# Kernel tuning notes

Measured on AMD Instinct MI355X. Metric: run time of the kernel, lower is better.

The kernel has to match this reference:

```python
import math
import jax, jax.numpy as jnp
import numpy as np

B, L, D, H, V, R, NL = 4, 1024, 1024, 16, 50257, 4, 3
LORA_SCALE = 32.0 / R  # alpha / r
EPS = 1e-5
GELU_C = math.sqrt(2.0 / math.pi)


def gelu(x):
    return 0.5 * x * (1.0 + jnp.tanh(GELU_C * (x + 0.044715 * x ** 3)))


def layer_norm(x, w, b):
    u = x.mean(-1, keepdims=True)
    s = ((x - u) ** 2).mean(-1, keepdims=True)
    return w * (x - u) / jnp.sqrt(s + EPS) + b


def setup_inputs() -> dict:
    key = jax.random.key(0)
    ks = jax.random.split(key, 10)
    std = 0.02
    inp = {
        'input_ids': jax.random.randint(ks[0], (B, L), 0, V),
        'wte': jax.random.normal(ks[1], (V, D), jnp.float32) * std,
        'wpe': jax.random.normal(ks[2], (L, D), jnp.float32) * std,
        'ln1_w': jnp.ones((NL, D), jnp.float32),
        'ln1_b': jnp.zeros((NL, D), jnp.float32),
        'attn_w': jax.random.normal(ks[3], (NL, D, 3 * D), jnp.float32) * std,
        'attn_b': jnp.zeros((NL, 3 * D), jnp.float32),
        'lora_A': jax.random.normal(ks[4], (NL, 2 * R, D), jnp.float32) * std,
        'lora_B': jax.random.normal(ks[5], (NL, 2 * D, R), jnp.float32) * std,
        'proj_w': jax.random.normal(ks[6], (NL, D, D), jnp.float32) * std,
        'proj_b': jnp.zeros((NL, D), jnp.float32),
        'ln2_w': jnp.ones((NL, D), jnp.float32),
        'ln2_b': jnp.zeros((NL, D), jnp.float32),
        'fc_w': jax.random.normal(ks[7], (NL, D, 4 * D), jnp.float32) * std,
        'fc_b': jnp.zeros((NL, 4 * D), jnp.float32),
        'fc2_w': jax.random.normal(ks[8], (NL, 4 * D, D), jnp.float32) * std,
        'fc2_b': jnp.zeros((NL, D), jnp.float32),
    }
    return inp


def block(x, causal, p):
    (ln1w, ln1b, aw, ab, lA, lB, pw, pb, ln2w, ln2b, fw, fb, f2w, f2b) = p
    h = layer_norm(x, ln1w, ln1b)
    # LoRA-merged QKV: base GEMM + low-rank deltas on Q and V groups
    qkv = h @ aw + ab                     # [B,L,3D]
    after_A = h @ lA.T                    # [B,L,2R]
    dq = after_A[..., :R] @ lB[:D].T * LORA_SCALE   # [B,L,D]
    dv = after_A[..., R:] @ lB[D:].T * LORA_SCALE   # [B,L,D]
    q = qkv[..., :D] + dq
    k = qkv[..., D:2 * D]
    v = qkv[..., 2 * D:] + dv
    # split heads -> [B,H,L,hd]
    hd = D // H
    q = q.reshape(B, L, H, hd).transpose(0, 2, 1, 3)
    k = k.reshape(B, L, H, hd).transpose(0, 2, 1, 3)
    v = v.reshape(B, L, H, hd).transpose(0, 2, 1, 3)
    w = jnp.einsum('bhqd,bhkd->bhqk', q, k) / math.sqrt(hd)
    w = w * causal - 1e10 * (1.0 - causal)  # multiplicative causal mask trick
    w = jax.nn.softmax(w, axis=-1)
    a = jnp.einsum('bhqk,bhkd->bhqd', w, v)
    a = a.transpose(0, 2, 1, 3).reshape(B, L, D)
    a = a @ pw + pb
    x = x + a
    m = layer_norm(x, ln2w, ln2b)
    m = gelu(m @ fw + fb) @ f2w + f2b
    return x + m


def reference(input_ids, wte, wpe, ln1_w, ln1_b, attn_w, attn_b, lora_A, lora_B,
              proj_w, proj_b, ln2_w, ln2_b, fc_w, fc_b, fc2_w, fc2_b):
    pos = jnp.arange(L)
    x = wte[input_ids] + wpe[pos][None, :, :]   # [B,L,D]
    causal = jnp.tril(jnp.ones((L, L), x.dtype))
    for i in range(NL):
        p = (ln1_w[i], ln1_b[i], attn_w[i], attn_b[i], lora_A[i], lora_B[i],
             proj_w[i], proj_b[i], ln2_w[i], ln2_b[i], fc_w[i], fc_b[i],
             fc2_w[i], fc2_b[i])
        x = block(x, causal, p)
    return x
```

## Files before the change

### kernel.cpp

```cpp
#include <hip/hip_runtime.h>

typedef __bf16 bf16x8 __attribute__((ext_vector_type(8)));
typedef float f32x4 __attribute__((ext_vector_type(4)));
typedef unsigned short u16x8 __attribute__((ext_vector_type(8)));
typedef unsigned short u16x4 __attribute__((ext_vector_type(4)));
typedef unsigned int u32x4 __attribute__((ext_vector_type(4)));

#define DEV static __device__ __forceinline__

DEV unsigned short f2bf(float f){
  return __builtin_bit_cast(unsigned short, (__bf16)f);
}
DEV float bf2f(unsigned short h){
  return __builtin_bit_cast(float, ((unsigned int)h) << 16);
}
DEV f32x4 bf4_to_f32(u16x4 h){
  f32x4 r = {bf2f(h[0]), bf2f(h[1]), bf2f(h[2]), bf2f(h[3])};
  return r;
}
DEV float gelu_f(float x){
  float z = 0.7978845608028654f * (x + 0.044715f * x * x * x);
  float e = __expf(2.0f * z);
  float th = 1.0f - 2.0f / (e + 1.0f);
  return 0.5f * x * (1.0f + th);
}

#define BAR() do{ asm volatile("" ::: "memory"); __builtin_amdgcn_s_barrier(); asm volatile("" ::: "memory"); }while(0)
#define LGKM0() asm volatile("s_waitcnt lgkmcnt(0)" ::: "memory")

__global__ __launch_bounds__(256)
void prep_weights(const float* __restrict__ attnw, const float* __restrict__ lorA,
                  const float* __restrict__ lorB, const float* __restrict__ projw,
                  const float* __restrict__ fcw, const float* __restrict__ fc2w,
                  unsigned short* __restrict__ WTA, unsigned short* __restrict__ WTP,
                  unsigned short* __restrict__ WTF, unsigned short* __restrict__ WTF2){
  __shared__ float tile[32][33];
  const int blk = blockIdx.x;
  const int layer = blk / 12288;
  const int r = blk % 12288;
  const float* in; unsigned short* out; int R, C, bx, by; bool lora;
  if (r < 3072){
    in = attnw + (size_t)layer*1024*3072; out = WTA + (size_t)layer*3072*1024;
    R = 1024; C = 3072; bx = r % 96; by = r / 96; lora = true;
  } else if (r < 4096){
    int rr = r - 3072;
    in = projw + (size_t)layer*1024*1024; out = WTP + (size_t)layer*1024*1024;
    R = 1024; C = 1024; bx = rr % 32; by = rr / 32; lora = false;
  } else if (r < 8192){
    int rr = r - 4096;
    in = fcw + (size_t)layer*1024*4096; out = WTF + (size_t)layer*4096*1024;
    R = 1024; C = 4096; bx = rr % 128; by = rr / 128; lora = false;
  } else {
    int rr = r - 8192;
    in = fc2w + (size_t)layer*4096*1024; out = WTF2 + (size_t)layer*1024*4096;
    R = 4096; C = 1024; bx = rr % 32; by = rr / 32; lora = false;
  }
  const int t = threadIdx.x;
  const int tx = t & 31, ty = t >> 5;
  const int r0 = by * 32, c0 = bx * 32;
  int seg = 0;
  f32x4 lb = {0.f, 0.f, 0.f, 0.f};
  const float* lA = nullptr;
  if (lora){
    seg = (c0 < 1024) ? 0 : ((c0 >= 2048) ? 2 : 1);
    if (seg != 1){
      int c = c0 + tx;
      int lbrow = (seg == 0) ? c : (c - 1024);
      lb = *(const f32x4*)(lorB + (size_t)layer*8192 + (size_t)lbrow*4);
      lA = lorA + (size_t)layer*8192 + ((seg == 0) ? 0 : 4096);
    }
  }
  #pragma unroll
  for (int kk = 0; kk < 4; ++kk){
    int krow = r0 + ty + kk*8;
    float v = in[(size_t)krow * C + c0 + tx];
    if (lora && seg != 1){
      v += 8.0f * (lA[krow]*lb[0] + lA[1024 + krow]*lb[1] +
                   lA[2048 + krow]*lb[2] + lA[3072 + krow]*lb[3]);
    }
    if (lora && seg == 1) v *= 0.125f;
    tile[ty + kk*8][tx] = v;
  }
  __syncthreads();
  const int orow = t >> 3, oc4 = (t & 7) * 4;
  u16x4 ov;
  #pragma unroll
  for (int c = 0; c < 4; ++c) ov[c] = f2bf(tile[oc4 + c][orow]);
  *(u16x4*)(out + (size_t)(c0 + orow) * R + r0 + oc4) = ov;
}

DEV void ln_finish(f32x4 v, const float* __restrict__ wgt,
                   const float* __restrict__ bia, unsigned short* __restrict__ out,
                   int m, int t, float* red){
  float s  = v[0] + v[1] + v[2] + v[3];
  float ss = v[0]*v[0] + v[1]*v[1] + v[2]*v[2] + v[3]*v[3];
  #pragma unroll
  for (int off = 32; off >= 1; off >>= 1){
    s  += __shfl_xor(s, off);
    ss += __shfl_xor(ss, off);
  }
  if ((t & 63) == 0){ red[(t>>6)*2] = s; red[(t>>6)*2+1] = ss; }
  __syncthreads();
  float S  = red[0] + red[2] + red[4] + red[6];
  float SS = red[1] + red[3] + red[5] + red[7];
  float mean = S * (1.0f/1024.0f);
  float var  = SS * (1.0f/1024.0f) - mean*mean;
  float rstd = rsqrtf(var + 1e-5f);
  f32x4 wv = *(const f32x4*)(wgt + t*4);
  f32x4 bv = *(const f32x4*)(bia + t*4);
  u16x4 o;
  #pragma unroll
  for (int j = 0; j < 4; ++j) o[j] = f2bf(wv[j] * (v[j] - mean) * rstd + bv[j]);
  *(u16x4*)(out + (size_t)m * 1024 + t*4) = o;
}

__global__ __launch_bounds__(256)
void embed_ln(const int* __restrict__ ids, const float* __restrict__ wte,
              const float* __restrict__ wpe, const float* __restrict__ wgt,
              const float* __restrict__ bia, float* __restrict__ x,
              unsigned short* __restrict__ hb){
  __shared__ float red[8];
  const int m = blockIdx.x, t = threadIdx.x;
  const int id = ids[m], lpos = m & 1023;
  f32x4 a = *(const f32x4*)(wte + (size_t)id * 1024 + t*4);
  f32x4 p = *(const f32x4*)(wpe + (size_t)lpos * 1024 + t*4);
  f32x4 v = a + p;
  *(f32x4*)(x + (size_t)m * 1024 + t*4) = v;
  ln_finish(v, wgt, bia, hb, m, t, red);
}

__global__ __launch_bounds__(256)
void ln_kernel(const float* __restrict__ x, const float* __restrict__ wgt,
               const float* __restrict__ bia, unsigned short* __restrict__ out){
  __shared__ float red[8];
  const int m = blockIdx.x, t = threadIdx.x;
  f32x4 v = *(const f32x4*)(x + (size_t)m * 1024 + t*4);
  ln_finish(v, wgt, bia, out, m, t, red);
}

__global__ __launch_bounds__(256)
void reduce_ln(const unsigned short* __restrict__ P, const float* __restrict__ res,
               const float* __restrict__ bias, float* __restrict__ xout,
               const float* __restrict__ wgt, const float* __restrict__ bia,
               unsigned short* __restrict__ hb){
  __shared__ float red[8];
  const int m = blockIdx.x, t = threadIdx.x;
  const size_t off = (size_t)m*1024 + t*4;
  const size_t MN = (size_t)4096*1024;
  f32x4 v = bf4_to_f32(*(const u16x4*)(P + off));
  v += bf4_to_f32(*(const u16x4*)(P + MN + off));
  v += bf4_to_f32(*(const u16x4*)(P + 2*MN + off));
  v += bf4_to_f32(*(const u16x4*)(P + 3*MN + off));
  v += *(const f32x4*)(res + off);
  v += *(const f32x4*)(bias + t*4);
  *(f32x4*)(xout + off) = v;
  ln_finish(v, wgt, bia, hb, m, t, red);
}

__global__ __launch_bounds__(256)
void fc2_reduce(const unsigned short* __restrict__ P, const float* __restrict__ res,
                const float* __restrict__ bias, float* __restrict__ out){
  const int m = blockIdx.x, t = threadIdx.x;
  const size_t off = (size_t)m*1024 + t*4;
  const size_t MN = (size_t)4096*1024;
  f32x4 v = bf4_to_f32(*(const u16x4*)(P + off));
  v += bf4_to_f32(*(const u16x4*)(P + MN + off));
  v += bf4_to_f32(*(const u16x4*)(P + 2*MN + off));
  v += bf4_to_f32(*(const u16x4*)(P + 3*MN + off));
  v += *(const f32x4*)(res + off);
  v += *(const f32x4*)(bias + t*4);
  *(f32x4*)(out + off) = v;
}

template<int MODE>
__global__ __launch_bounds__(512, 1)
void gemm256(const unsigned short* __restrict__ A,
             const unsigned short* __restrict__ Wt,
             const float* __restrict__ bias,
             void* __restrict__ outp, void* __restrict__ outp2,
             int M, int N, int K, int ldk){
  extern __shared__ char sm[];
  const int t = threadIdx.x, w = t >> 6, l = t & 63, g = l >> 4, q = l & 15;
  const int wr = w >> 2, wc = w & 3;
  const int gx = gridDim.x;
  const int nwg = gx * gridDim.y;
  const int id  = blockIdx.x + gx * blockIdx.y;
  const int id2 = (id & 7) * (nwg >> 3) + (id >> 3);
  const int bm = (id2 / gx) * 256, bn = (id2 % gx) * 256;
  const int koff = blockIdx.z * K;
  const int NT = K >> 6;
  const int sr = t >> 3, sc = (t & 7) ^ (sr & 7);
  __attribute__((address_space(3))) char* smAS = (__attribute__((address_space(3))) char*)sm;

#define STAGE_A(slot, qd, tile) do{ \
    const unsigned short* _s = A + (size_t)(bm + (qd)*64 + sr)*ldk + koff + ((tile)<<6) + sc*8; \
    __builtin_amdgcn_global_load_lds((const __attribute__((address_space(1))) void*)_s, \
      (__attribute__((address_space(3))) void*)(smAS + (slot)*32768 + (qd)*8192 + t*16), 16, 0, 0); }while(0)
#define STAGE_B(slot, qd, tile) do{ \
    const unsigned short* _s = Wt + (size_t)(bn + (qd)*64 + sr)*ldk + koff + ((tile)<<6) + sc*8; \
    __builtin_amdgcn_global_load_lds((const __attribute__((address_space(1))) void*)_s, \
      (__attribute__((address_space(3))) void*)(smAS + 65536 + (slot)*32768 + (qd)*8192 + t*16), 16, 0, 0); }while(0)

  const int arow = (wr*128 + q) * 128;
  const int brow = (wc*64  + q) * 128;
  const int c0 = ((g    ) ^ (q & 7)) << 4;
  const int c1 = ((4 + g) ^ (q & 7)) << 4;

  f32x4 acc[8][4];
  #pragma unroll
  for (int m = 0; m < 8; ++m)
    #pragma unroll
    for (int n = 0; n < 4; ++n) acc[m][n] = (f32x4){0.f,0.f,0.f,0.f};

  STAGE_A(0,0,0); STAGE_A(0,1,0); STAGE_A(0,2,0); STAGE_A(0,3,0);
  STAGE_B(0,0,0); STAGE_B(0,1,0); STAGE_B(0,2,0); STAGE_B(0,3,0);
  if (NT > 1){
    STAGE_B(1,0,1); STAGE_B(1,1,1); STAGE_B(1,2,1); STAGE_B(1,3,1);
    STAGE_A(1,0,1); STAGE_A(1,2,1);
    asm volatile("s_waitcnt vmcnt(6)" ::: "memory");
  } else {
    asm volatile("s_waitcnt vmcnt(0)" ::: "memory");
  }
  BAR();

  u16x8 bk0[4], bk1[4];
  for (int T = 0; T < NT; ++T){
    const int cur = T & 1, nxt = cur ^ 1;
    const int curA = cur*32768, curB = 65536 + cur*32768;
    if (T + 1 < NT){ STAGE_A(nxt, 1, T+1); STAGE_A(nxt, 3, T+1); }
    u16x8 a00 = *(const u16x8*)(sm + curA + arow + 0*2048 + c0);
    u16x8 a01 = *(const u16x8*)(sm + curA + arow + 0*2048 + c1);
    u16x8 a10 = *(const u16x8*)(sm + curA + arow + 1*2048 + c0);
    u16x8 a11 = *(const u16x8*)(sm + curA + arow + 1*2048 + c1);
    #pragma unroll
    for (int n = 0; n < 4; ++n){
      bk0[n] = *(const u16x8*)(sm + curB + brow + n*2048 + c0);
      bk1[n] = *(const u16x8*)(sm + curB + brow + n*2048 + c1);
    }
    BAR(); LGKM0();
    __builtin_amdgcn_s_setprio(1);
    #pragma unroll
    for (int n = 0; n < 4; ++n){
      acc[0][n] = __builtin_amdgcn_mfma_f32_16x16x32_bf16(__builtin_bit_cast(bf16x8,a00), __builtin_bit_cast(bf16x8,bk0[n]), acc[0][n], 0,0,0);
      acc[0][n] = __builtin_amdgcn_mfma_f32_16x16x32_bf16(__builtin_bit_cast(bf16x8,a01), __builtin_bit_cast(bf16x8,bk1[n]), acc[0][n], 0,0,0);
      acc[1][n] = __builtin_amdgcn_mfma_f32_16x16x32_bf16(__builtin_bit_cast(bf16x8,a10), __builtin_bit_cast(bf16x8,bk0[n]), acc[1][n], 0,0,0);
      acc[1][n] = __builtin_amdgcn_mfma_f32_16x16x32_bf16(__builtin_bit_cast(bf16x8,a11), __builtin_bit_cast(bf16x8,bk1[n]), acc[1][n], 0,0,0);
    }
    __builtin_amdgcn_s_setprio(0);
    BAR();
    if (T + 2 < NT){ STAGE_B(cur, 0, T+2); STAGE_B(cur, 1, T+2); }
    a00 = *(const u16x8*)(sm + curA + arow + 2*2048 + c0);
    a01 = *(const u16x8*)(sm + curA + arow + 2*2048 + c1);
    a10 = *(const u16x8*)(sm + curA + arow + 3*2048 + c0);
    a11 = *(const u16x8*)(sm + curA + arow + 3*2048 + c1);
    BAR(); LGKM0();
    __builtin_amdgcn_s_setprio(1);
    #pragma unroll
    for (int n = 0; n < 4; ++n){
      acc[2][n] = __builtin_amdgcn_mfma_f32_16x16x32_bf16(__builtin_bit_cast(bf16x8,a00), __builtin_bit_cast(bf16x8,bk0[n]), acc[2][n], 0,0,0);
      acc[2][n] = __builtin_amdgcn_mfma_f32_16x16x32_bf16(__builtin_bit_cast(bf16x8,a01), __builtin_bit_cast(bf16x8,bk1[n]), acc[2][n], 0,0,0);
      acc[3][n] = __builtin_amdgcn_mfma_f32_16x16x32_bf16(__builtin_bit_cast(bf16x8,a10), __builtin_bit_cast(bf16x8,bk0[n]), acc[3][n], 0,0,0);
      acc[3][n] = __builtin_amdgcn_mfma_f32_16x16x32_bf16(__builtin_bit_cast(bf16x8,a11), __builtin_bit_cast(bf16x8,bk1[n]), acc[3][n], 0,0,0);
    }
    __builtin_amdgcn_s_setprio(0);
    BAR();
    if (T + 2 < NT){ STAGE_B(cur, 2, T+2); STAGE_B(cur, 3, T+2); STAGE_A(cur, 0, T+2); STAGE_A(cur, 2, T+2); }
    a00 = *(const u16x8*)(sm + curA + arow + 4*2048 + c0);
    a01 = *(const u16x8*)(sm + curA + arow + 4*2048 + c1);
    a10 = *(const u16x8*)(sm + curA + arow + 5*2048 + c0);
    a11 = *(const u16x8*)(sm + curA + arow + 5*2048 + c1);
    BAR(); LGKM0();
    __builtin_amdgcn_s_setprio(1);
    #pragma unroll
    for (int n = 0; n < 4; ++n){
      acc[4][n] = __builtin_amdgcn_mfma_f32_16x16x32_bf16(__builtin_bit_cast(bf16x8,a00), __builtin_bit_cast(bf16x8,bk0[n]), acc[4][n], 0,0,0);
      acc[4][n] = __builtin_amdgcn_mfma_f32_16x16x32_bf16(__builtin_bit_cast(bf16x8,a01), __builtin_bit_cast(bf16x8,bk1[n]), acc[4][n], 0,0,0);
      acc[5][n] = __builtin_amdgcn_mfma_f32_16x16x32_bf16(__builtin_bit_cast(bf16x8,a10), __builtin_bit_cast(bf16x8,bk0[n]), acc[5][n], 0,0,0);
      acc[5][n] = __builtin_amdgcn_mfma_f32_16x16x32_bf16(__builtin_bit_cast(bf16x8,a11), __builtin_bit_cast(bf16x8,bk1[n]), acc[5][n], 0,0,0);
    }
    __builtin_amdgcn_s_setprio(0);
    BAR();
    a00 = *(const u16x8*)(sm + curA + arow + 6*2048 + c0);
    a01 = *(const u16x8*)(sm + curA + arow + 6*2048 + c1);
    a10 = *(const u16x8*)(sm + curA + arow + 7*2048 + c0);
    a11 = *(const u16x8*)(sm + curA + arow + 7*2048 + c1);
    if (T + 2 < NT){ asm volatile("s_waitcnt vmcnt(6)" ::: "memory"); }
    else if (T + 1 < NT){ asm volatile("s_waitcnt vmcnt(0)" ::: "memory"); }
    BAR(); LGKM0();
    __builtin_amdgcn_s_setprio(1);
    #pragma unroll
    for (int n = 0; n < 4; ++n){
      acc[6][n] = __builtin_amdgcn_mfma_f32_16x16x32_bf16(__builtin_bit_cast(bf16x8,a00), __builtin_bit_cast(bf16x8,bk0[n]), acc[6][n], 0,0,0);
      acc[6][n] = __builtin_amdgcn_mfma_f32_16x16x32_bf16(__builtin_bit_cast(bf16x8,a01), __builtin_bit_cast(bf16x8,bk1[n]), acc[6][n], 0,0,0);
      acc[7][n] = __builtin_amdgcn_mfma_f32_16x16x32_bf16(__builtin_bit_cast(bf16x8,a10), __builtin_bit_cast(bf16x8,bk0[n]), acc[7][n], 0,0,0);
      acc[7][n] = __builtin_amdgcn_mfma_f32_16x16x32_bf16(__builtin_bit_cast(bf16x8,a11), __builtin_bit_cast(bf16x8,bk1[n]), acc[7][n], 0,0,0);
    }
    __builtin_amdgcn_s_setprio(0);
    BAR();
  }
#undef STAGE_A
#undef STAGE_B
  unsigned short* pout4 = (MODE == 4) ? ((unsigned short*)outp + (size_t)blockIdx.z * M * N) : nullptr;
  #pragma unroll
  for (int n = 0; n < 4; ++n){
    int col = bn + wc*64 + n*16 + q;
    float bv = (MODE == 4) ? 0.f : bias[col];
    if (MODE == 5 && (col >> 10) == 1) bv *= 0.125f;
    #pragma unroll
    for (int m = 0; m < 8; ++m){
      int row0 = bm + wr*128 + m*16 + g*4;
      if (MODE == 5 && col >= 2048){
        int dh = col & 63, hh = (col >> 6) & 15;
        int bb = row0 >> 10, ll = row0 & 1023;
        u16x4 pv;
        #pragma unroll
        for (int r = 0; r < 4; ++r) pv[r] = f2bf(acc[m][n][r] + bv);
        *(u16x4*)((unsigned short*)outp2 + ((size_t)(bb*16 + hh)*64 + dh)*1024 + ll) = pv;
      } else {
        #pragma unroll
        for (int r = 0; r < 4; ++r){
          float v = acc[m][n][r] + bv;
          if (MODE == 2){
            ((unsigned short*)outp)[(size_t)(row0 + r)*N + col] = f2bf(gelu_f(v));
          } else if (MODE == 5){
            ((unsigned short*)outp)[(size_t)(row0 + r)*N + col] = f2bf(v);
          } else if (MODE == 4){
            pout4[(size_t)(row0 + r)*N + col] = f2bf(v);
          }
        }
      }
    }
  }
}

template<int MODE>
__global__ __launch_bounds__(256)
void gemm_bf16(const unsigned short* __restrict__ A,
               const unsigned short* __restrict__ Wt,
               const float* __restrict__ bias,
               const float* __restrict__ res,
               void* __restrict__ outp,
               int M, int N, int K){
  __shared__ unsigned short As[128*32];
  __shared__ unsigned short Bs[128*32];
  const int t = threadIdx.x;
  const int w = t >> 6, l = t & 63;
  const int wr = w >> 1, wc = w & 1;
  const int g = l >> 4, q = l & 15;
  const int gxn = gridDim.x;
  const int nwg = gxn * gridDim.y;
  const int bid = blockIdx.x + gxn * blockIdx.y;
  const int bid2 = ((nwg & 7) == 0) ? ((bid & 7)*(nwg >> 3) + (bid >> 3)) : bid;
  const int bm = (bid2 / gxn) * 128, bn = (bid2 % gxn) * 128;
  const int srow = t >> 2, schunk = t & 3;
  const unsigned short* Ag = A  + (size_t)(bm + srow)*K + schunk*8;
  const unsigned short* Bg = Wt + (size_t)(bn + srow)*K + schunk*8;
  const int sa0 = srow*64        + ((schunk ^ ((srow>>1)&3)) << 4);
  const int sa1 = (srow+64)*64   + ((schunk ^ (((srow+64)>>1)&3)) << 4);
  f32x4 acc[4][4];
  #pragma unroll
  for (int m = 0; m < 4; ++m)
    #pragma unroll
    for (int n = 0; n < 4; ++n) acc[m][n] = (f32x4){0.f,0.f,0.f,0.f};
  const int nk = K >> 5;
  u16x8 ra0 = *(const u16x8*)(Ag);
  u16x8 ra1 = *(const u16x8*)(Ag + (size_t)64*K);
  u16x8 rb0 = *(const u16x8*)(Bg);
  u16x8 rb1 = *(const u16x8*)(Bg + (size_t)64*K);
  for (int kt = 0; kt < nk; ++kt){
    __syncthreads();
    *(u16x8*)((char*)As + sa0) = ra0;
    *(u16x8*)((char*)As + sa1) = ra1;
    *(u16x8*)((char*)Bs + sa0) = rb0;
    *(u16x8*)((char*)Bs + sa1) = rb1;
    __syncthreads();
    if (kt + 1 < nk){
      const unsigned short* A2 = Ag + (size_t)(kt+1)*32;
      const unsigned short* B2 = Bg + (size_t)(kt+1)*32;
      ra0 = *(const u16x8*)(A2);
      ra1 = *(const u16x8*)(A2 + (size_t)64*K);
      rb0 = *(const u16x8*)(B2);
      rb1 = *(const u16x8*)(B2 + (size_t)64*K);
    }
    bf16x8 af[4], bfr[4];
    #pragma unroll
    for (int m = 0; m < 4; ++m){
      int row = wr*64 + m*16 + q;
      af[m] = __builtin_bit_cast(bf16x8,
        *(const u16x8*)((char*)As + row*64 + ((g ^ ((row>>1)&3)) << 4)));
    }
    #pragma unroll
    for (int n = 0; n < 4; ++n){
      int row = wc*64 + n*16 + q;
      bfr[n] = __builtin_bit_cast(bf16x8,
        *(const u16x8*)((char*)Bs + row*64 + ((g ^ ((row>>1)&3)) << 4)));
    }
    #pragma unroll
    for (int m = 0; m < 4; ++m)
      #pragma unroll
      for (int n = 0; n < 4; ++n)
        acc[m][n] = __builtin_amdgcn_mfma_f32_16x16x32_bf16(af[m], bfr[n], acc[m][n], 0, 0, 0);
  }
  #pragma unroll
  for (int n = 0; n < 4; ++n){
    int col = bn + wc*64 + n*16 + q;
    float bv = bias[col];
    #pragma unroll
    for (int m = 0; m < 4; ++m){
      int row0 = bm + wr*64 + m*16 + g*4;
      #pragma unroll
      for (int r = 0; r < 4; ++r){
        int row = row0 + r;
        float v = acc[m][n][r] + bv;
        if (MODE == 1) v += res[(size_t)row*N + col];
        if (MODE == 2){
          ((unsigned short*)outp)[(size_t)row*N + col] = f2bf(gelu_f(v));
        } else {
          ((float*)outp)[(size_t)row*N + col] = v;
        }
      }
    }
  }
}

__global__ __launch_bounds__(256)
void attn_kernel(const unsigned short* __restrict__ qkv,
                 const unsigned short* __restrict__ Vt,
                 unsigned short* __restrict__ Aout){
  __shared__ unsigned short Ks[64*64];
  __shared__ unsigned short Vs[64*64];
  const int t = threadIdx.x, w = t >> 6, l = t & 63, g = l >> 4, q = l & 15;
  const int qb = blockIdx.x, bh = blockIdx.y;
  const int b = bh >> 4, h = bh & 15;
  const size_t vbase = (size_t)bh * 65536;
  const int qrow = qb*64 + w*16 + q;
  const unsigned short* Qr = qkv + (size_t)(b*1024 + qrow)*3072 + h*64;
  bf16x8 qf0 = __builtin_bit_cast(bf16x8, *(const u16x8*)(Qr + g*8));
  bf16x8 qf1 = __builtin_bit_cast(bf16x8, *(const u16x8*)(Qr + 32 + g*8));
  f32x4 o[4];
  #pragma unroll
  for (int d = 0; d < 4; ++d) o[d] = (f32x4){0.f,0.f,0.f,0.f};
  float mprev = -1e30f, lsum = 0.f;
  const int srow = t >> 3, schunk = t & 7;
  const int nkt = qb + 1;
  u16x8 kvr[2], vvr[2];
  #pragma unroll
  for (int it = 0; it < 2; ++it){
    int r = srow + it*32;
    kvr[it] = *(const u16x8*)(qkv + (size_t)(b*1024 + r)*3072 + 1024 + h*64 + schunk*8);
    vvr[it] = *(const u16x8*)(Vt + vbase + (size_t)r*1024 + schunk*8);
  }
  for (int kt = 0; kt < nkt; ++kt){
    __syncthreads();
    #pragma unroll
    for (int it = 0; it < 2; ++it){
      int r = srow + it*32;
      *(u16x8*)((char*)Ks + r*128 + ((schunk ^ (r&7)) << 4)) = kvr[it];
      *(u16x8*)((char*)Vs + r*128 + ((schunk ^ (r&7)) << 4)) = vvr[it];
    }
    __syncthreads();
    if (kt + 1 < nkt){
      const int k1 = (kt + 1) * 64;
      #pragma unroll
      for (int it = 0; it < 2; ++it){
        int r = srow + it*32;
        kvr[it] = *(const u16x8*)(qkv + (size_t)(b*1024 + k1 + r)*3072 + 1024 + h*64 + schunk*8);
        vvr[it] = *(const u16x8*)(Vt + vbase + (size_t)r*1024 + k1 + schunk*8);
      }
    }
    const int k0 = kt * 64;
    f32x4 st[4];
    #pragma unroll
    for (int kf = 0; kf < 4; ++kf) st[kf] = (f32x4){0.f,0.f,0.f,0.f};
    #pragma unroll
    for (int kf = 0; kf < 4; ++kf){
      int krow = kf*16 + q;
      bf16x8 k0f = __builtin_bit_cast(bf16x8,
        *(const u16x8*)((char*)Ks + krow*128 + ((g       ^ (krow&7)) << 4)));
      bf16x8 k1f = __builtin_bit_cast(bf16x8,
        *(const u16x8*)((char*)Ks + krow*128 + (((4 + g) ^ (krow&7)) << 4)));
      st[kf] = __builtin_amdgcn_mfma_f32_16x16x32_bf16(k0f, qf0, st[kf], 0, 0, 0);
      st[kf] = __builtin_amdgcn_mfma_f32_16x16x32_bf16(k1f, qf1, st[kf], 0, 0, 0);
    }
    if (kt == nkt - 1){
      #pragma unroll
      for (int kf = 0; kf < 4; ++kf)
        #pragma unroll
        for (int r = 0; r < 4; ++r){
          int kg = k0 + kf*16 + g*4 + r;
          if (kg > qrow) st[kf][r] = -1e30f;
        }
    }
    float tmax = -1e30f;
    #pragma unroll
    for (int kf = 0; kf < 4; ++kf)
      #pragma unroll
      for (int r = 0; r < 4; ++r) tmax = fmaxf(tmax, st[kf][r]);
    tmax = fmaxf(tmax, __shfl_xor(tmax, 16));
    tmax = fmaxf(tmax, __shfl_xor(tmax, 32));
    float mnew = fmaxf(mprev, tmax);
    float p[4][4]; float tsum = 0.f;
    #pragma unroll
    for (int kf = 0; kf < 4; ++kf)
      #pragma unroll
      for (int r = 0; r < 4; ++r){
        float e = __expf(st[kf][r] - mnew);
        p[kf][r] = e; tsum += e;
      }
    tsum += __shfl_xor(tsum, 16);
    tsum += __shfl_xor(tsum, 32);
    float alpha = __expf(mprev - mnew);
    lsum = lsum * alpha + tsum;
    mprev = mnew;
    float al0 = __shfl(alpha, 20*g + 0);
    float al1 = __shfl(alpha, 20*g + 1);
    float al2 = __shfl(alpha, 20*g + 2);
    float al3 = __shfl(alpha, 20*g + 3);
    #pragma unroll
    for (int d = 0; d < 4; ++d){
      o[d][0] *= al0; o[d][1] *= al1; o[d][2] *= al2; o[d][3] *= al3;
    }
    unsigned pk0[4], pk1[4];
    #pragma unroll
    for (int kf = 0; kf < 4; ++kf){
      pk0[kf] = (unsigned)f2bf(p[kf][0]) | ((unsigned)f2bf(p[kf][1]) << 16);
      pk1[kf] = (unsigned)f2bf(p[kf][2]) | ((unsigned)f2bf(p[kf][3]) << 16);
    }
    const int sa = (((g & 1) << 1) << 4) | q;
    const int sb = ((((g & 1) << 1) | 1) << 4) | q;
    const bool hi2 = (g >= 2);
    #pragma unroll
    for (int ks = 0; ks < 2; ++ks){
      const int kA = 2*ks, kB = 2*ks + 1;
      unsigned a0 = (unsigned)__shfl((int)pk0[kA], sa);
      unsigned b0 = (unsigned)__shfl((int)pk0[kB], sa);
      unsigned a1 = (unsigned)__shfl((int)pk1[kA], sa);
      unsigned b1 = (unsigned)__shfl((int)pk1[kB], sa);
      unsigned a2 = (unsigned)__shfl((int)pk0[kA], sb);
      unsigned b2 = (unsigned)__shfl((int)pk0[kB], sb);
      unsigned a3 = (unsigned)__shfl((int)pk1[kA], sb);
      unsigned b3 = (unsigned)__shfl((int)pk1[kB], sb);
      u32x4 pw = { hi2 ? b0 : a0, hi2 ? b1 : a1, hi2 ? b2 : a2, hi2 ? b3 : a3 };
      bf16x8 pa = __builtin_bit_cast(bf16x8, pw);
      #pragma unroll
      for (int df = 0; df < 4; ++df){
        int vrow = df*16 + q;
        bf16x8 vf = __builtin_bit_cast(bf16x8,
          *(const u16x8*)((char*)Vs + vrow*128 + (((ks*4 + g) ^ (vrow&7)) << 4)));
        o[df] = __builtin_amdgcn_mfma_f32_16x16x32_bf16(pa, vf, o[df], 0, 0, 0);
      }
    }
  }
  float r0 = 1.f / __shfl(lsum, 20*g + 0);
  float r1 = 1.f / __shfl(lsum, 20*g + 1);
  float r2 = 1.f / __shfl(lsum, 20*g + 2);
  float r3 = 1.f / __shfl(lsum, 20*g + 3);
  const int orow0 = qb*64 + w*16 + g*4;
  #pragma unroll
  for (int df = 0; df < 4; ++df){
    int col = h*64 + df*16 + q;
    Aout[((size_t)(b*1024 + orow0 + 0))*1024 + col] = f2bf(o[df][0] * r0);
    Aout[((size_t)(b*1024 + orow0 + 1))*1024 + col] = f2bf(o[df][1] * r1);
    Aout[((size_t)(b*1024 + orow0 + 2))*1024 + col] = f2bf(o[df][2] * r2);
    Aout[((size_t)(b*1024 + orow0 + 3))*1024 + col] = f2bf(o[df][3] * r3);
  }
}

extern "C" void kernel_launch(void* const* d_in, const int* in_sizes, int n_in,
                              void* d_out, int out_size, void* d_ws, size_t ws_size,
                              hipStream_t stream){
  (void)in_sizes; (void)n_in; (void)out_size; (void)ws_size;
  const int*   ids   = (const int*)  d_in[0];
  const float* wte   = (const float*)d_in[1];
  const float* wpe   = (const float*)d_in[2];
  const float* ln1w  = (const float*)d_in[3];
  const float* ln1b  = (const float*)d_in[4];
  const float* attnw = (const float*)d_in[5];
  const float* attnb = (const float*)d_in[6];
  const float* lorA  = (const float*)d_in[7];
  const float* lorB  = (const float*)d_in[8];
  const float* projw = (const float*)d_in[9];
  const float* projb = (const float*)d_in[10];
  const float* ln2w  = (const float*)d_in[11];
  const float* ln2b  = (const float*)d_in[12];
  const float* fcw   = (const float*)d_in[13];
  const float* fcb   = (const float*)d_in[14];
  const float* fc2w  = (const float*)d_in[15];
  const float* fc2b  = (const float*)d_in[16];

  char* p = (char*)d_ws;
  float* XA  = (float*)p;                    p += 16777216;
  float* XB  = (float*)p;                    p += 16777216;
  unsigned short* HB   = (unsigned short*)p; p += 8388608;
  unsigned short* MBf  = (unsigned short*)p; p += 8388608;
  unsigned short* QKVb = (unsigned short*)p; p += 25165824;
  unsigned short* Vtb  = (unsigned short*)p; p += 8388608;
  unsigned short* AO   = (unsigned short*)p; p += 8388608;
  unsigned short* ACT  = (unsigned short*)p; p += 33554432;
  unsigned short* PSUM = (unsigned short*)p; p += 33554432;
  unsigned short* WTA  = (unsigned short*)p; p += 18874368;
  unsigned short* WTP  = (unsigned short*)p; p += 6291456;
  unsigned short* WTF  = (unsigned short*)p; p += 25165824;
  unsigned short* WTF2 = (unsigned short*)p; p += 25165824;

  prep_weights<<<36864, 256, 0, stream>>>(attnw, lorA, lorB, projw, fcw, fc2w,
                                          WTA, WTP, WTF, WTF2);
  embed_ln<<<4096, 256, 0, stream>>>(ids, wte, wpe, ln1w, ln1b, XA, HB);

  for (int i = 0; i < 3; ++i){
    gemm256<5><<<dim3(12, 16), 512, 131072, stream>>>(HB, WTA + (size_t)i*3072*1024, attnb + i*3072, QKVb, Vtb, 4096, 3072, 1024, 1024);
    attn_kernel<<<dim3(16, 64), 256, 0, stream>>>(QKVb, Vtb, AO);
    gemm_bf16<1><<<dim3(8, 32), 256, 0, stream>>>(AO, WTP + (size_t)i*1024*1024, projb + i*1024, XA, XB, 4096, 1024, 1024);
    ln_kernel<<<4096, 256, 0, stream>>>(XB, ln2w + i*1024, ln2b + i*1024, MBf);
    gemm256<2><<<dim3(16, 16), 512, 131072, stream>>>(MBf, WTF + (size_t)i*4096*1024, fcb + i*4096, ACT, nullptr, 4096, 4096, 1024, 1024);
    gemm256<4><<<dim3(4, 16, 4), 512, 131072, stream>>>(ACT, WTF2 + (size_t)i*1024*4096, nullptr, PSUM, nullptr, 4096, 1024, 1024, 4096);
    if (i < 2){
      reduce_ln<<<4096, 256, 0, stream>>>(PSUM, XB, fc2b + i*1024, XA,
                                          ln1w + (i+1)*1024, ln1b + (i+1)*1024, HB);
    } else {
      fc2_reduce<<<4096, 256, 0, stream>>>(PSUM, XB, fc2b + i*1024, (float*)d_out);
    }
  }
}
```

Before: 681.9 us.

## Enlarge attention query tile to 128 rows with 8 waves per block

The attention kernel now handles 128 query rows per block using 512 threads (8 waves), so each K/V tile staged in shared memory is reused by twice as many query rows. Each thread stages one 16-byte chunk per tile instead of two. Waves whose query rows lie entirely before a K tile skip that tile's compute. The causal mask is now applied per wave instead of only on the last tile. The grid is halved. In exchange, the waves in a block finish at different times, so some idle at barriers on the diagonal tiles, and there are fewer blocks to fill the device.

New measurement: 670.0 us. About the same (-1.7%).

```diff
diff --git a/kernel.cpp b/kernel.cpp
--- a/kernel.cpp
+++ b/kernel.cpp
@@ -423,7 +423,7 @@
   }
 }
 
-__global__ __launch_bounds__(256)
+__global__ __launch_bounds__(512)
 void attn_kernel(const unsigned short* __restrict__ qkv,
                  const unsigned short* __restrict__ Vt,
                  unsigned short* __restrict__ Aout){
@@ -433,7 +433,8 @@
   const int qb = blockIdx.x, bh = blockIdx.y;
   const int b = bh >> 4, h = bh & 15;
   const size_t vbase = (size_t)bh * 65536;
-  const int qrow = qb*64 + w*16 + q;
+  const int qrow = qb*128 + w*16 + q;
+  const int wq_hi = qb*128 + w*16 + 15;
   const unsigned short* Qr = qkv + (size_t)(b*1024 + qrow)*3072 + h*64;
   bf16x8 qf0 = __builtin_bit_cast(bf16x8, *(const u16x8*)(Qr + g*8));
   bf16x8 qf1 = __builtin_bit_cast(bf16x8, *(const u16x8*)(Qr + 32 + g*8));
@@ -442,33 +443,22 @@
   for (int d = 0; d < 4; ++d) o[d] = (f32x4){0.f,0.f,0.f,0.f};
   float mprev = -1e30f, lsum = 0.f;
   const int srow = t >> 3, schunk = t & 7;
-  const int nkt = qb + 1;
-  u16x8 kvr[2], vvr[2];
-  #pragma unroll
-  for (int it = 0; it < 2; ++it){
-    int r = srow + it*32;
-    kvr[it] = *(const u16x8*)(qkv + (size_t)(b*1024 + r)*3072 + 1024 + h*64 + schunk*8);
-    vvr[it] = *(const u16x8*)(Vt + vbase + (size_t)r*1024 + schunk*8);
-  }
+  const int nkt = 2*qb + 2;
+  u16x8 kvr, vvr;
+  kvr = *(const u16x8*)(qkv + (size_t)(b*1024 + srow)*3072 + 1024 + h*64 + schunk*8);
+  vvr = *(const u16x8*)(Vt + vbase + (size_t)srow*1024 + schunk*8);
   for (int kt = 0; kt < nkt; ++kt){
     __syncthreads();
-    #pragma unroll
-    for (int it = 0; it < 2; ++it){
-      int r = srow + it*32;
-      *(u16x8*)((char*)Ks + r*128 + ((schunk ^ (r&7)) << 4)) = kvr[it];
-      *(u16x8*)((char*)Vs + r*128 + ((schunk ^ (r&7)) << 4)) = vvr[it];
-    }
+    *(u16x8*)((char*)Ks + srow*128 + ((schunk ^ (srow&7)) << 4)) = kvr;
+    *(u16x8*)((char*)Vs + srow*128 + ((schunk ^ (srow&7)) << 4)) = vvr;
     __syncthreads();
     if (kt + 1 < nkt){
       const int k1 = (kt + 1) * 64;
-      #pragma unroll
-      for (int it = 0; it < 2; ++it){
-        int r = srow + it*32;
-        kvr[it] = *(const u16x8*)(qkv + (size_t)(b*1024 + k1 + r)*3072 + 1024 + h*64 + schunk*8);
-        vvr[it] = *(const u16x8*)(Vt + vbase + (size_t)r*1024 + k1 + schunk*8);
-      }
+      kvr = *(const u16x8*)(qkv + (size_t)(b*1024 + k1 + srow)*3072 + 1024 + h*64 + schunk*8);
+      vvr = *(const u16x8*)(Vt + vbase + (size_t)srow*1024 + k1 + schunk*8);
     }
     const int k0 = kt * 64;
+    if (k0 > wq_hi) continue;
     f32x4 st[4];
     #pragma unroll
     for (int kf = 0; kf < 4; ++kf) st[kf] = (f32x4){0.f,0.f,0.f,0.f};
@@ -482,7 +472,7 @@
       st[kf] = __builtin_amdgcn_mfma_f32_16x16x32_bf16(k0f, qf0, st[kf], 0, 0, 0);
       st[kf] = __builtin_amdgcn_mfma_f32_16x16x32_bf16(k1f, qf1, st[kf], 0, 0, 0);
     }
-    if (kt == nkt - 1){
+    if (k0 + 63 > qrow){
       #pragma unroll
       for (int kf = 0; kf < 4; ++kf)
         #pragma unroll
@@ -555,7 +545,7 @@
   float r1 = 1.f / __shfl(lsum, 20*g + 1);
   float r2 = 1.f / __shfl(lsum, 20*g + 2);
   float r3 = 1.f / __shfl(lsum, 20*g + 3);
-  const int orow0 = qb*64 + w*16 + g*4;
+  const int orow0 = qb*128 + w*16 + g*4;
   #pragma unroll
   for (int df = 0; df < 4; ++df){
     int col = h*64 + df*16 + q;
@@ -609,7 +599,7 @@
 
   for (int i = 0; i < 3; ++i){
     gemm256<5><<<dim3(12, 16), 512, 131072, stream>>>(HB, WTA + (size_t)i*3072*1024, attnb + i*3072, QKVb, Vtb, 4096, 3072, 1024, 1024);
-    attn_kernel<<<dim3(16, 64), 256, 0, stream>>>(QKVb, Vtb, AO);
+    attn_kernel<<<dim3(8, 64), 512, 0, stream>>>(QKVb, Vtb, AO);
     gemm_bf16<1><<<dim3(8, 32), 256, 0, stream>>>(AO, WTP + (size_t)i*1024*1024, projb + i*1024, XA, XB, 4096, 1024, 1024);
     ln_kernel<<<4096, 256, 0, stream>>>(XB, ln2w + i*1024, ln2b + i*1024, MBf);
     gemm256<2><<<dim3(16, 16), 512, 131072, stream>>>(MBf, WTF + (size_t)i*4096*1024, fcb + i*4096, ACT, nullptr, 4096, 4096, 1024, 1024);
```
